# Performance work log

Hardware: AMD Instinct MI355X
Metric: run time of the kernel (lower is better)

Reference implementation:

```python
import jax, jax.numpy as jnp
import numpy as np

T, B, D, H, R, S, M = 1024, 16, 512, 8, 32, 16, 16
TQ = R + T + S   # query length
KL = M + R + T   # key/value length
NEG_INF = -1e8


def setup_inputs() -> dict:
    key = jax.random.key(0)
    ks = jax.random.split(key, 12)
    utterance = jax.random.normal(ks[0], (T, B, D), jnp.float32)
    right_context = jax.random.normal(ks[1], (R, B, D), jnp.float32)
    summary = jax.random.normal(ks[2], (S, B, D), jnp.float32)
    mems = jax.random.normal(ks[3], (M, B, D), jnp.float32)
    # valid lengths in [T//2, T]; force max == T so data-dependent shapes are static
    lengths = jax.random.randint(ks[4], (B,), T // 2, T + 1).at[0].set(T).astype(jnp.int64)
    # block-streaming style mask: query i may only attend to keys <= i + M
    q_idx = jnp.arange(TQ)[:, None]
    k_idx = jnp.arange(KL)[None, :]
    attention_mask = k_idx > (q_idx + M)  # True = masked
    scale = 0.02
    Wq = jax.random.normal(ks[5], (D, D), jnp.float32) * scale
    bq = jnp.zeros((D,), jnp.float32)
    Wkv = jax.random.normal(ks[6], (2 * D, D), jnp.float32) * scale
    bkv = jnp.zeros((2 * D,), jnp.float32)
    Wo = jax.random.normal(ks[7], (D, D), jnp.float32) * scale
    bo = jnp.zeros((D,), jnp.float32)
    return dict(utterance=utterance, lengths=lengths, right_context=right_context,
                summary=summary, mems=mems, attention_mask=attention_mask,
                Wq=Wq, bq=bq, Wkv=Wkv, bkv=bkv, Wo=Wo, bo=bo)


def _split_heads(x):
    # (L, B, D) -> (B*H, L, D//H), matching torch .view(-1, B*H, d).transpose(0, 1)
    L = x.shape[0]
    return x.reshape(L, B * H, D // H).transpose(1, 0, 2)


def reference(utterance, lengths, right_context, summary, mems, attention_mask,
              Wq, bq, Wkv, bkv, Wo, bo):
    d_head = D // H
    scaling = d_head ** -0.5

    query_in = jnp.concatenate([right_context, utterance, summary], axis=0)   # (TQ, B, D)
    kv_in = jnp.concatenate([mems, right_context, utterance], axis=0)         # (KL, B, D)

    query = query_in @ Wq.T + bq
    kv = kv_in @ Wkv.T + bkv
    k, v = jnp.split(kv, 2, axis=2)

    q = _split_heads(query)  # (B*H, TQ, d)
    kh = _split_heads(k)     # (B*H, KL, d)
    vh = _split_heads(v)

    w = jnp.einsum('nqd,nkd->nqk', q * scaling, kh).astype(jnp.float32)
    w = jnp.where(attention_mask[None, :, :], NEG_INF, w)

    # padding mask (B > 1 path): klengths = lengths + M + right_context_blocks_length
    rcbl = TQ - jnp.max(lengths) - S  # == R since max(lengths) == T
    klengths = lengths + M + rcbl
    pad_mask = jnp.arange(KL)[None, :] >= klengths[:, None]  # (B, KL)
    w = w.reshape(B, H, TQ, KL)
    w = jnp.where(pad_mask[:, None, None, :], NEG_INF, w)
    w = w.reshape(B * H, TQ, KL)

    probs = jax.nn.softmax(w, axis=-1)  # dropout p=0.0
    attn = jnp.einsum('nqk,nkd->nqd', probs, vh)          # (B*H, TQ, d)
    attn = attn.transpose(1, 0, 2).reshape(TQ, B, D)

    out = attn @ Wo.T + bo                                # (TQ, B, D)
    output_right_context = out[:TQ - S]                    # (R+T, B, D)
    output_mems = jnp.clip(out[TQ - S:], -10.0, 10.0)      # tanh_on_mem=False
    return output_right_context, output_mems[:-1]          # (S-1, B, D)
```

## Files before the change

### kernel.cpp

```cpp
#include <hip/hip_runtime.h>

#define T_   1024
#define B_   16
#define D_   512
#define H_   8
#define R_   32
#define S_   16
#define M_   16
#define TQ_  1072
#define KL_  1072
#define DH_  64
#define NROW 17152
#define K_   512
#define LQ_  268
#define QSCALE 0.18033688f

typedef unsigned short u16;
using bf16x8 = __attribute__((ext_vector_type(8))) short;
using f32x4  = __attribute__((ext_vector_type(4))) float;
using u16x4  = __attribute__((ext_vector_type(4))) unsigned short;

__device__ __forceinline__ u16 f2bf(float f) {
    unsigned int u = __builtin_bit_cast(unsigned int, f);
    unsigned int r = u + 0x7fffu + ((u >> 16) & 1u);
    return (u16)(r >> 16);
}

__device__ __forceinline__ unsigned int cvt_pk_bf16(float a, float b) {
    unsigned int r;
    asm("v_cvt_pk_bf16_f32 %0, %1, %2" : "=v"(r) : "v"(a), "v"(b));
    return r;
}

__device__ __forceinline__ void gload_lds16(const u16* g, u16* l) {
    __builtin_amdgcn_global_load_lds(
        (const __attribute__((address_space(1))) unsigned int*)g,
        (__attribute__((address_space(3))) unsigned int*)l,
        16, 0, 0);
}

__global__ void k_convert4(const float4* __restrict__ utt, const float4* __restrict__ rc,
                           const float4* __restrict__ smr, const float4* __restrict__ mems,
                           const float4* __restrict__ Wq, const float4* __restrict__ Wkv,
                           const float4* __restrict__ Wo,
                           u16x4* __restrict__ xall,
                           u16x4* __restrict__ wq, u16x4* __restrict__ wkv,
                           u16x4* __restrict__ wo)
{
    const int N4 = 17408 * D_ / 4;
    const int MB = M_ * B_ * D_ / 4;
    const int RB = MB + R_ * B_ * D_ / 4;
    const int UB = RB + T_ * B_ * D_ / 4;
    const int W1 = D_ * D_ / 4, W2 = 2 * D_ * D_ / 4;
    for (int i = blockIdx.x * blockDim.x + threadIdx.x; i < N4;
         i += gridDim.x * blockDim.x) {
        float4 v;
        if (i < MB)      v = mems[i];
        else if (i < RB) v = rc[i - MB];
        else if (i < UB) v = utt[i - RB];
        else             v = smr[i - UB];
        xall[i] = (u16x4){f2bf(v.x), f2bf(v.y), f2bf(v.z), f2bf(v.w)};
        if (i < W1) { v = Wq[i];  wq[i]  = (u16x4){f2bf(v.x), f2bf(v.y), f2bf(v.z), f2bf(v.w)}; }
        if (i < W2) { v = Wkv[i]; wkv[i] = (u16x4){f2bf(v.x), f2bf(v.y), f2bf(v.z), f2bf(v.w)}; }
        if (i < W1) { v = Wo[i];  wo[i]  = (u16x4){f2bf(v.x), f2bf(v.y), f2bf(v.z), f2bf(v.w)}; }
    }
}

#define GEMM_SHARED                                                              \
    __shared__ __align__(16) u16 As[256 * 64];                                   \
    __shared__ __align__(16) u16 Bs[128 * 64];

#define GEMM_PRE(A_PTR, W_PTR)                                                   \
    const int w    = threadIdx.x >> 6;                                           \
    const int lane = threadIdx.x & 63;                                           \
    const int col = lane & 15, quad = lane >> 4;                                 \
    const int lrow = lane >> 3;                                        \
    const int lchk = (lane & 7) ^ lrow;                      \
    const u16* gA = (A_PTR) + (size_t)(tm * 256 + w * 64 + lrow) * K_ + lchk * 8;\
    const u16* gB = (W_PTR) + (size_t)(w * 32 + lrow) * K_ + lchk * 8;

#define GEMM_STAGE(k0)                                                           \
        __syncthreads();                                                         \
        _Pragma("unroll")                                                        \
        for (int i = 0; i < 8; i++)                                              \
            gload_lds16(gA + (k0) + (size_t)i * 8 * K_,                          \
                        &As[(w * 64 + i * 8) * 64]);                             \
        _Pragma("unroll")                                                        \
        for (int j = 0; j < 4; j++)                                              \
            gload_lds16(gB + (k0) + (size_t)j * 8 * K_,                          \
                        &Bs[(w * 32 + j * 8) * 64]);                             \
        __syncthreads();

#define GEMM_FRAGS(kh)                                                           \
            bf16x8 aF[4], bF[8];                                                 \
            _Pragma("unroll")                                                    \
            for (int mi = 0; mi < 4; mi++)                                       \
                aF[mi] = *(const bf16x8*)&As[(w * 64 + mi * 16 + col) * 64       \
                             + ((((kh) * 4 + quad) ^ (col & 7)) * 8)];           \
            _Pragma("unroll")                                                    \
            for (int ni = 0; ni < 8; ni++)                                       \
                bF[ni] = *(const bf16x8*)&Bs[(ni * 16 + col) * 64                \
                             + ((((kh) * 4 + quad) ^ (col & 7)) * 8)];

#define GEMM_CORE(A_PTR, W_PTR)                                                  \
    GEMM_PRE(A_PTR, W_PTR)                                                       \
    f32x4 acc[4][8];                                                             \
    _Pragma("unroll")                                                            \
    for (int mi = 0; mi < 4; mi++)                                               \
        _Pragma("unroll")                                                        \
        for (int ni = 0; ni < 8; ni++) acc[mi][ni] = (f32x4){0.f,0.f,0.f,0.f};   \
    for (int k0 = 0; k0 < K_; k0 += 64) {                                        \
        GEMM_STAGE(k0)                                                           \
        _Pragma("unroll")                                                        \
        for (int kh = 0; kh < 2; kh++) {                                         \
            GEMM_FRAGS(kh)                                                       \
            _Pragma("unroll")                                                    \
            for (int mi = 0; mi < 4; mi++)                                       \
                _Pragma("unroll")                                                \
                for (int ni = 0; ni < 8; ni++)                                   \
                    acc[mi][ni] = __builtin_amdgcn_mfma_f32_16x16x32_bf16(       \
                                      aF[mi], bF[ni], acc[mi][ni], 0, 0, 0);     \
        }                                                                        \
    }

#define GEMM_CORE_T(A_PTR, W_PTR)                                                \
    GEMM_PRE(A_PTR, W_PTR)                                                       \
    f32x4 acc[8][4];                                                             \
    _Pragma("unroll")                                                            \
    for (int ni = 0; ni < 8; ni++)                                               \
        _Pragma("unroll")                                                        \
        for (int mi = 0; mi < 4; mi++) acc[ni][mi] = (f32x4){0.f,0.f,0.f,0.f};   \
    for (int k0 = 0; k0 < K_; k0 += 64) {                                        \
        GEMM_STAGE(k0)                                                           \
        _Pragma("unroll")                                                        \
        for (int kh = 0; kh < 2; kh++) {                                         \
            GEMM_FRAGS(kh)                                                       \
            _Pragma("unroll")                                                    \
            for (int ni = 0; ni < 8; ni++)                                       \
                _Pragma("unroll")                                                \
                for (int mi = 0; mi < 4; mi++)                                   \
                    acc[ni][mi] = __builtin_amdgcn_mfma_f32_16x16x32_bf16(       \
                                      bF[ni], aF[mi], acc[ni][mi], 0, 0, 0);     \
        }                                                                        \
    }

__global__ __launch_bounds__(256, 2)
void k_gemm_qkv(const u16* __restrict__ xall,
                const u16* __restrict__ wqp, const u16* __restrict__ wkvp,
                const float* __restrict__ bq, const float* __restrict__ bkv,
                u16* __restrict__ qb, u16* __restrict__ kb, u16* __restrict__ vt)
{
    const int bid = blockIdx.x;
    const int tn = (bid % 96) >> 3;
    const int tm = (bid / 96) * 8 + (bid & 7);
    if (tm >= 67) return;

    const bool isQ = tn < 4;
    const bool isV = tn >= 8;
    const int wr0 = (isQ ? tn : tn - 4) * 128;
    const u16* Ab = isQ ? (xall + (size_t)256 * K_) : xall;
    const u16* Wb = (isQ ? wqp : wkvp) + (size_t)wr0 * K_;
    const float* bias = isQ ? bq : bkv;

    GEMM_SHARED

    if (isV) {
        GEMM_CORE(Ab, Wb)
#pragma unroll
        for (int ni = 0; ni < 8; ni++) {
            int gcol = wr0 + ni * 16 + col;
            float bs = bias[gcol];
            int f  = gcol - 512;
            int lq = tm * 4 + w;
#pragma unroll
            for (int r = 0; r < 4; r++) {
                int bb = quad * 4 + r;
                uint2 pk;
                pk.x = cvt_pk_bf16(acc[0][ni][r] + bs, acc[1][ni][r] + bs);
                pk.y = cvt_pk_bf16(acc[2][ni][r] + bs, acc[3][ni][r] + bs);
                *(uint2*)&vt[(((size_t)bb * LQ_ + lq) * 512 + f) * 4] = pk;
            }
        }
    } else {
        GEMM_CORE_T(Ab, Wb)
#pragma unroll
        for (int ni = 0; ni < 8; ni++) {
            const int gc0 = wr0 + ni * 16 + quad * 4;
            const float4 bs4 = *(const float4*)&bias[gc0];
#pragma unroll
            for (int mi = 0; mi < 4; mi++) {
                const int mrow = tm * 256 + w * 64 + mi * 16 + col;
                uint2 pk;
                if (isQ) {
                    pk.x = cvt_pk_bf16((acc[ni][mi][0] + bs4.x) * QSCALE,
                                       (acc[ni][mi][1] + bs4.y) * QSCALE);
                    pk.y = cvt_pk_bf16((acc[ni][mi][2] + bs4.z) * QSCALE,
                                       (acc[ni][mi][3] + bs4.w) * QSCALE);
                    *(uint2*)&qb[(size_t)mrow * 512 + gc0] = pk;
                } else {
                    pk.x = cvt_pk_bf16(acc[ni][mi][0] + bs4.x,
                                       acc[ni][mi][1] + bs4.y);
                    pk.y = cvt_pk_bf16(acc[ni][mi][2] + bs4.z,
                                       acc[ni][mi][3] + bs4.w);
                    *(uint2*)&kb[(size_t)mrow * 512 + gc0] = pk;
                }
            }
        }
    }
}

__global__ __launch_bounds__(256, 2)
void k_gemm_o(const u16* __restrict__ A, const u16* __restrict__ W,
              const float* __restrict__ bias, float* __restrict__ Co)
{
    const int bid = blockIdx.x;
    const int tn = (bid % 32) >> 3;
    const int tm = (bid / 32) * 8 + (bid & 7);
    if (tm >= 67) return;

    const u16* Wb = W + (size_t)tn * 128 * K_;

    GEMM_SHARED
    GEMM_CORE_T(A, Wb)

#pragma unroll
    for (int ni = 0; ni < 8; ni++) {
        const int gc0 = tn * 128 + ni * 16 + quad * 4;
        const float4 bs4 = *(const float4*)&bias[gc0];
#pragma unroll
        for (int mi = 0; mi < 4; mi++) {
            const int l = tm * 16 + w * 4 + mi;
            if (l == TQ_ - 1) continue;
            const int mrow = tm * 256 + w * 64 + mi * 16 + col;
            float4 v = {acc[ni][mi][0] + bs4.x, acc[ni][mi][1] + bs4.y,
                        acc[ni][mi][2] + bs4.z, acc[ni][mi][3] + bs4.w};
            if (l >= TQ_ - S_) {
                v.x = fminf(10.0f, fmaxf(-10.0f, v.x));
                v.y = fminf(10.0f, fmaxf(-10.0f, v.y));
                v.z = fminf(10.0f, fmaxf(-10.0f, v.z));
                v.w = fminf(10.0f, fmaxf(-10.0f, v.w));
            }
            *(float4*)&Co[(size_t)mrow * 512 + gc0] = v;
        }
    }
}

__global__ __launch_bounds__(256, 2)
void k_attn5(const u16* __restrict__ qbuf, const u16* __restrict__ kb,
             const u16* __restrict__ vt, const int* __restrict__ lenp,
             u16* __restrict__ attnb)
{
    __shared__ __align__(16) u16 Ks[2][64 * 64];
    __shared__ __align__(16) u16 Vs[2][64 * 64];
    __shared__ __align__(16) u16 Ps[4][16 * 64];

    const int blk  = blockIdx.x;
    const int qblk = 16 - (blk >> 7);
    const int bh   = blk & 127;
    const int b = bh >> 3, h = bh & 7;
    const int tid = threadIdx.x;
    const int w = tid >> 6, lane = tid & 63;
    const int col = lane & 15, quad = lane >> 4;

    int stride = (lenp[1] == 0) ? 2 : 1;
    int maxlen = 0;
    for (int i = 0; i < B_; i++) maxlen = max(maxlen, lenp[i * stride]);
    const int klen = lenp[b * stride] + M_ + (TQ_ - maxlen - S_);

    const int q0 = qblk * 64;
    const int qw = q0 + w * 16;
    const int q  = qw + col;

    int qrow = min(q, TQ_ - 1);
    const u16* qp = qbuf + ((size_t)qrow * B_ + b) * D_ + h * DH_ + quad * 8;
    bf16x8 bq0 = *(const bf16x8*)(qp);
    bf16x8 bq1 = *(const bf16x8*)(qp + 32);

    const int s0 = tid, s1 = tid + 256;
    const u16* kbase = kb + (size_t)b * 512 + h * DH_;
    size_t kof0 = (size_t)(s0 >> 3) * 8192 + (size_t)(((s0 & 7) ^ ((s0 >> 3) & 7)) * 8);
    size_t kof1 = (size_t)(s1 >> 3) * 8192 + (size_t)(((s1 & 7) ^ ((s1 >> 3) & 7)) * 8);
    const u16* vbase = vt + ((size_t)b * LQ_ * 512 + (size_t)h * DH_) * 4;
    auto vchunk = [](int s) -> size_t {
        int fp = s >> 4;
        int lq = (s & 15) ^ (fp & 15);
        return (size_t)lq * 2048 + (size_t)fp * 8;
    };
    const size_t vof0 = vchunk(s0), vof1 = vchunk(s1);

    float li = 0.f;
    f32x4 o[4];
#pragma unroll
    for (int g = 0; g < 4; g++) o[g] = (f32x4){0.f, 0.f, 0.f, 0.f};

    const int nk = min(q0 + 64 + M_, klen);
    const int numkt = (nk + 63) >> 6;
    u16* pw = &Ps[w][0];

    gload_lds16(kbase + kof0, &Ks[0][(size_t)w * 512]);
    gload_lds16(kbase + kof1, &Ks[0][2048 + (size_t)w * 512]);
    gload_lds16(vbase + vof0, &Vs[0][(size_t)w * 512]);
    gload_lds16(vbase + vof1, &Vs[0][2048 + (size_t)w * 512]);

    for (int kt = 0; kt < numkt; kt++) {
        const int kn0 = kt * 64;
        const int cur = kt & 1;
        __syncthreads();
        if (kt + 1 < numkt) {
            const size_t kstep = (size_t)(kn0 + 64) * 8192;
            const size_t vstep = (size_t)(kt + 1) * 32768;
            gload_lds16(kbase + kstep + kof0, &Ks[cur ^ 1][(size_t)w * 512]);
            gload_lds16(kbase + kstep + kof1, &Ks[cur ^ 1][2048 + (size_t)w * 512]);
            gload_lds16(vbase + vstep + vof0, &Vs[cur ^ 1][(size_t)w * 512]);
            gload_lds16(vbase + vstep + vof1, &Vs[cur ^ 1][2048 + (size_t)w * 512]);
        }

        f32x4 sc[4];
        __builtin_amdgcn_s_setprio(1);
#pragma unroll
        for (int g = 0; g < 4; g++) {
            int key = g * 16 + col;
            bf16x8 a0 = *(const bf16x8*)&Ks[cur][key * 64 + ((quad ^ (key & 7)) * 8)];
            bf16x8 a1 = *(const bf16x8*)&Ks[cur][key * 64 + (((4 + quad) ^ (key & 7)) * 8)];
            f32x4 z = {0.f, 0.f, 0.f, 0.f};
            z = __builtin_amdgcn_mfma_f32_16x16x32_bf16(a0, bq0, z, 0, 0, 0);
            z = __builtin_amdgcn_mfma_f32_16x16x32_bf16(a1, bq1, z, 0, 0, 0);
            sc[g] = z;
        }
        __builtin_amdgcn_s_setprio(0);

        const bool needmask = (kn0 + 63 > qw + M_) || (kn0 + 63 >= klen);
        if (needmask) {
#pragma unroll
            for (int g = 0; g < 4; g++)
#pragma unroll
                for (int r = 0; r < 4; r++) {
                    int key = kn0 + g * 16 + quad * 4 + r;
                    bool valid = (key <= q + M_) && (key < klen);
                    sc[g][r] = valid ? sc[g][r] : -1e8f;
                }
        }

#pragma unroll
        for (int g = 0; g < 4; g++) {
            float pr[4];
#pragma unroll
            for (int r = 0; r < 4; r++) {
                pr[r] = __builtin_amdgcn_exp2f(sc[g][r]);
                li += pr[r];
            }
            uint2 pk;
            pk.x = cvt_pk_bf16(pr[0], pr[1]);
            pk.y = cvt_pk_bf16(pr[2], pr[3]);
            int kc = g * 2 + (quad >> 1);
            *(uint2*)&pw[col * 64 + ((kc ^ (col & 7)) * 8) + (quad & 1) * 4] = pk;
        }

        bf16x8 ap0 = *(const bf16x8*)&pw[col * 64 + ((quad ^ (col & 7)) * 8)];
        bf16x8 ap1 = *(const bf16x8*)&pw[col * 64 + (((4 + quad) ^ (col & 7)) * 8)];
        __builtin_amdgcn_s_setprio(1);
#pragma unroll
        for (int g = 0; g < 4; g++) {
            int d = g * 16 + col;
            int fp = d >> 1, fo = (d & 1) * 4;
            bf16x8 bv[2];
#pragma unroll
            for (int hh = 0; hh < 2; hh++) {
                int lqA = hh * 8 + quad * 2;
                int posA = fp * 16 + (lqA ^ (fp & 15));
                int posB = fp * 16 + ((lqA + 1) ^ (fp & 15));
                u16x4 loA = *(const u16x4*)&Vs[cur][posA * 8 + fo];
                u16x4 loB = *(const u16x4*)&Vs[cur][posB * 8 + fo];
                bf16x8 t;
                t[0] = loA[0]; t[1] = loA[1]; t[2] = loA[2]; t[3] = loA[3];
                t[4] = loB[0]; t[5] = loB[1]; t[6] = loB[2]; t[7] = loB[3];
                bv[hh] = t;
            }
            o[g] = __builtin_amdgcn_mfma_f32_16x16x32_bf16(bv[0], ap0, o[g], 0, 0, 0);
            o[g] = __builtin_amdgcn_mfma_f32_16x16x32_bf16(bv[1], ap1, o[g], 0, 0, 0);
        }
        __builtin_amdgcn_s_setprio(0);
    }

    li += __shfl_xor(li, 16);
    li += __shfl_xor(li, 32);
    const float inv = 1.0f / li;
    const int qo = qw + col;
    if (qw + 16 <= TQ_) {
#pragma unroll
        for (int g = 0; g < 4; g++) {
            uint2 pk;
            pk.x = cvt_pk_bf16(o[g][0] * inv, o[g][1] * inv);
            pk.y = cvt_pk_bf16(o[g][2] * inv, o[g][3] * inv);
            *(uint2*)&attnb[((size_t)qo * B_ + b) * D_ + h * DH_ + g * 16 + quad * 4] = pk;
        }
    }
}

extern "C" void kernel_launch(void* const* d_in, const int* in_sizes, int n_in,
                              void* d_out, int out_size, void* d_ws, size_t ws_size,
                              hipStream_t stream)
{
    const float* utt  = (const float*)d_in[0];
    const int*   len  = (const int*)  d_in[1];
    const float* rc   = (const float*)d_in[2];
    const float* smr  = (const float*)d_in[3];
    const float* mems = (const float*)d_in[4];
    const float* Wq   = (const float*)d_in[6];
    const float* bq   = (const float*)d_in[7];
    const float* Wkv  = (const float*)d_in[8];
    const float* bkv  = (const float*)d_in[9];
    const float* Wo   = (const float*)d_in[10];
    const float* bo   = (const float*)d_in[11];

    char* ws = (char*)d_ws;
    size_t off = 0;
    auto alloc = [&](size_t bytes) -> void* {
        void* p = ws + off;
        off += (bytes + 255) & ~(size_t)255;
        return p;
    };
    u16* xall = (u16*)alloc((size_t)17408 * D_ * 2);
    u16* wq   = (u16*)alloc((size_t)D_ * D_ * 2);
    u16* wkv  = (u16*)alloc((size_t)2 * D_ * D_ * 2);
    u16* wo   = (u16*)alloc((size_t)D_ * D_ * 2);
    u16* qb   = (u16*)alloc((size_t)NROW * D_ * 2);
    u16* kb   = (u16*)alloc((size_t)NROW * D_ * 2);
    u16* vt   = (u16*)alloc((size_t)B_ * LQ_ * 512 * 4 * 2 + 65536);
    u16* attnb = xall;

    k_convert4<<<2048, 256, 0, stream>>>((const float4*)utt, (const float4*)rc,
                                         (const float4*)smr, (const float4*)mems,
                                         (const float4*)Wq, (const float4*)Wkv,
                                         (const float4*)Wo,
                                         (u16x4*)xall,
                                         (u16x4*)wq, (u16x4*)wkv, (u16x4*)wo);
    k_gemm_qkv<<<9 * 96, 256, 0, stream>>>(xall, wq, wkv, bq, bkv, qb, kb, vt);
    k_attn5<<<17 * 128, 256, 0, stream>>>(qb, kb, vt, len, attnb);
    k_gemm_o<<<9 * 32, 256, 0, stream>>>(attnb, wo, bo, (float*)d_out);
}
```

Before: 215.6 us.

## Rewrite projection GEMMs with double-buffered LDS pipeline and 8-wave 256x256 tiles

Both projection GEMMs move from a single-buffered 256x128 tile with 4 waves to a templated core that double-buffers A/B tiles in dynamic LDS and issues the next stage's loads before computing the current one. Blocks grow to 8 waves with 256x256 (QKV) or 128x256 (output) tiles, and MFMA sections are wrapped in s_setprio. The goal is to hide global-load latency behind MFMA work and cut redundant tile loads. In exchange it uses 128KB/96KB of LDS per block, which limits occupancy, and launches fewer blocks for the QKV GEMM (402).

```diff
diff --git a/kernel.cpp b/kernel.cpp
--- a/kernel.cpp
+++ b/kernel.cpp
@@ -66,174 +66,172 @@
     }
 }
 
-#define GEMM_SHARED                                                              \
-    __shared__ __align__(16) u16 As[256 * 64];                                   \
-    __shared__ __align__(16) u16 Bs[128 * 64];
-
-#define GEMM_PRE(A_PTR, W_PTR)                                                   \
-    const int w    = threadIdx.x >> 6;                                           \
-    const int lane = threadIdx.x & 63;                                           \
-    const int col = lane & 15, quad = lane >> 4;                                 \
-    const int lrow = lane >> 3;                                        \
-    const int lchk = (lane & 7) ^ lrow;                      \
-    const u16* gA = (A_PTR) + (size_t)(tm * 256 + w * 64 + lrow) * K_ + lchk * 8;\
-    const u16* gB = (W_PTR) + (size_t)(w * 32 + lrow) * K_ + lchk * 8;
-
-#define GEMM_STAGE(k0)                                                           \
-        __syncthreads();                                                         \
-        _Pragma("unroll")                                                        \
-        for (int i = 0; i < 8; i++)                                              \
-            gload_lds16(gA + (k0) + (size_t)i * 8 * K_,                          \
-                        &As[(w * 64 + i * 8) * 64]);                             \
-        _Pragma("unroll")                                                        \
-        for (int j = 0; j < 4; j++)                                              \
-            gload_lds16(gB + (k0) + (size_t)j * 8 * K_,                          \
-                        &Bs[(w * 32 + j * 8) * 64]);                             \
+template<int MREP, bool TOR>
+__device__ __forceinline__ void pipe_core(const u16* __restrict__ Ab,
+                                          const u16* __restrict__ Wb,
+                                          u16* lds, f32x4* acc)
+{
+    const int BM = MREP * 32;
+    u16* As0 = lds;
+    u16* As1 = lds + BM * 64;
+    u16* Bs0 = lds + 2 * BM * 64;
+    u16* Bs1 = lds + 2 * BM * 64 + 256 * 64;
+
+    const int tid  = threadIdx.x;
+    const int wid  = tid >> 6, lane = tid & 63;
+    const int wm   = wid >> 2, wn = wid & 3;
+    const int col  = lane & 15, quad = lane >> 4;
+    const int sr   = tid >> 3;
+    const int sc   = (tid & 7) ^ (sr & 7);
+    const u16* gA  = Ab + (size_t)sr * K_ + sc * 8;
+    const u16* gB  = Wb + (size_t)sr * K_ + sc * 8;
+
+#pragma unroll
+    for (int i = 0; i < MREP * 4; i++) acc[i] = (f32x4){0.f, 0.f, 0.f, 0.f};
+
+    auto stage = [&](int kt, u16* Au, u16* Bu) {
+#pragma unroll
+        for (int i = 0; i < MREP / 2; i++)
+            gload_lds16(gA + (size_t)(i * 64) * K_ + kt * 64,
+                        Au + (i * 64 + wid * 8) * 64);
+#pragma unroll
+        for (int i = 0; i < 4; i++)
+            gload_lds16(gB + (size_t)(i * 64) * K_ + kt * 64,
+                        Bu + (i * 64 + wid * 8) * 64);
+    };
+
+    stage(0, As0, Bs0);
+    __syncthreads();
+
+    u16 *Ac = As0, *Bc = Bs0, *An = As1, *Bn = Bs1;
+    for (int kt = 0; kt < 8; ++kt) {
+        if (kt < 7) stage(kt + 1, An, Bn);
+#pragma unroll
+        for (int kh = 0; kh < 2; ++kh) {
+            bf16x8 aF[MREP], bF[4];
+#pragma unroll
+            for (int mi = 0; mi < MREP; mi++)
+                aF[mi] = *(const bf16x8*)&Ac[(wm * (MREP * 16) + mi * 16 + col) * 64
+                             + (((kh * 4 + quad) ^ (col & 7)) * 8)];
+#pragma unroll
+            for (int ni = 0; ni < 4; ni++)
+                bF[ni] = *(const bf16x8*)&Bc[(wn * 64 + ni * 16 + col) * 64
+                             + (((kh * 4 + quad) ^ (col & 7)) * 8)];
+            __builtin_amdgcn_s_setprio(1);
+            if (TOR) {
+#pragma unroll
+                for (int ni = 0; ni < 4; ni++)
+#pragma unroll
+                    for (int mi = 0; mi < MREP; mi++)
+                        acc[ni * MREP + mi] = __builtin_amdgcn_mfma_f32_16x16x32_bf16(
+                            bF[ni], aF[mi], acc[ni * MREP + mi], 0, 0, 0);
+            } else {
+#pragma unroll
+                for (int mi = 0; mi < MREP; mi++)
+#pragma unroll
+                    for (int ni = 0; ni < 4; ni++)
+                        acc[mi * 4 + ni] = __builtin_amdgcn_mfma_f32_16x16x32_bf16(
+                            aF[mi], bF[ni], acc[mi * 4 + ni], 0, 0, 0);
+            }
+            __builtin_amdgcn_s_setprio(0);
+        }
         __syncthreads();
-
-#define GEMM_FRAGS(kh)                                                           \
-            bf16x8 aF[4], bF[8];                                                 \
-            _Pragma("unroll")                                                    \
-            for (int mi = 0; mi < 4; mi++)                                       \
-                aF[mi] = *(const bf16x8*)&As[(w * 64 + mi * 16 + col) * 64       \
-                             + ((((kh) * 4 + quad) ^ (col & 7)) * 8)];           \
-            _Pragma("unroll")                                                    \
-            for (int ni = 0; ni < 8; ni++)                                       \
-                bF[ni] = *(const bf16x8*)&Bs[(ni * 16 + col) * 64                \
-                             + ((((kh) * 4 + quad) ^ (col & 7)) * 8)];
-
-#define GEMM_CORE(A_PTR, W_PTR)                                                  \
-    GEMM_PRE(A_PTR, W_PTR)                                                       \
-    f32x4 acc[4][8];                                                             \
-    _Pragma("unroll")                                                            \
-    for (int mi = 0; mi < 4; mi++)                                               \
-        _Pragma("unroll")                                                        \
-        for (int ni = 0; ni < 8; ni++) acc[mi][ni] = (f32x4){0.f,0.f,0.f,0.f};   \
-    for (int k0 = 0; k0 < K_; k0 += 64) {                                        \
-        GEMM_STAGE(k0)                                                           \
-        _Pragma("unroll")                                                        \
-        for (int kh = 0; kh < 2; kh++) {                                         \
-            GEMM_FRAGS(kh)                                                       \
-            _Pragma("unroll")                                                    \
-            for (int mi = 0; mi < 4; mi++)                                       \
-                _Pragma("unroll")                                                \
-                for (int ni = 0; ni < 8; ni++)                                   \
-                    acc[mi][ni] = __builtin_amdgcn_mfma_f32_16x16x32_bf16(       \
-                                      aF[mi], bF[ni], acc[mi][ni], 0, 0, 0);     \
-        }                                                                        \
-    }
-
-#define GEMM_CORE_T(A_PTR, W_PTR)                                                \
-    GEMM_PRE(A_PTR, W_PTR)                                                       \
-    f32x4 acc[8][4];                                                             \
-    _Pragma("unroll")                                                            \
-    for (int ni = 0; ni < 8; ni++)                                               \
-        _Pragma("unroll")                                                        \
-        for (int mi = 0; mi < 4; mi++) acc[ni][mi] = (f32x4){0.f,0.f,0.f,0.f};   \
-    for (int k0 = 0; k0 < K_; k0 += 64) {                                        \
-        GEMM_STAGE(k0)                                                           \
-        _Pragma("unroll")                                                        \
-        for (int kh = 0; kh < 2; kh++) {                                         \
-            GEMM_FRAGS(kh)                                                       \
-            _Pragma("unroll")                                                    \
-            for (int ni = 0; ni < 8; ni++)                                       \
-                _Pragma("unroll")                                                \
-                for (int mi = 0; mi < 4; mi++)                                   \
-                    acc[ni][mi] = __builtin_amdgcn_mfma_f32_16x16x32_bf16(       \
-                                      bF[ni], aF[mi], acc[ni][mi], 0, 0, 0);     \
-        }                                                                        \
-    }
-
-__global__ __launch_bounds__(256, 2)
-void k_gemm_qkv(const u16* __restrict__ xall,
-                const u16* __restrict__ wqp, const u16* __restrict__ wkvp,
-                const float* __restrict__ bq, const float* __restrict__ bkv,
-                u16* __restrict__ qb, u16* __restrict__ kb, u16* __restrict__ vt)
-{
+        u16* t;
+        t = Ac; Ac = An; An = t;
+        t = Bc; Bc = Bn; Bn = t;
+    }
+}
+
+__global__ __launch_bounds__(512, 2)
+void k_gemm_qkv8(const u16* __restrict__ xall,
+                 const u16* __restrict__ wqp, const u16* __restrict__ wkvp,
+                 const float* __restrict__ bq, const float* __restrict__ bkv,
+                 u16* __restrict__ qb, u16* __restrict__ kb, u16* __restrict__ vt)
+{
+    extern __shared__ u16 lds[];
     const int bid = blockIdx.x;
-    const int tn = (bid % 96) >> 3;
-    const int tm = (bid / 96) * 8 + (bid & 7);
-    if (tm >= 67) return;
-
-    const bool isQ = tn < 4;
-    const bool isV = tn >= 8;
-    const int wr0 = (isQ ? tn : tn - 4) * 128;
-    const u16* Ab = isQ ? (xall + (size_t)256 * K_) : xall;
-    const u16* Wb = (isQ ? wqp : wkvp) + (size_t)wr0 * K_;
-    const float* bias = isQ ? bq : bkv;
-
-    GEMM_SHARED
-
-    if (isV) {
-        GEMM_CORE(Ab, Wb)
-#pragma unroll
-        for (int ni = 0; ni < 8; ni++) {
-            int gcol = wr0 + ni * 16 + col;
-            float bs = bias[gcol];
-            int f  = gcol - 512;
-            int lq = tm * 4 + w;
-#pragma unroll
-            for (int r = 0; r < 4; r++) {
-                int bb = quad * 4 + r;
+    const int tn = bid % 6, tm = bid / 6;
+    const int typ = tn >> 1, half = tn & 1;
+    const u16* Ab = (typ == 0 ? xall + (size_t)256 * K_ : xall)
+                    + (size_t)tm * 256 * K_;
+    const u16* Wb = (typ == 0 ? wqp : wkvp + (typ == 2 ? (size_t)512 * K_ : 0))
+                    + (size_t)half * 256 * K_;
+
+    const int wid = threadIdx.x >> 6, lane = threadIdx.x & 63;
+    const int wm = wid >> 2, wn = wid & 3;
+    const int col = lane & 15, quad = lane >> 4;
+
+    f32x4 acc[32];
+    if (typ == 2) {
+        pipe_core<8, false>(Ab, Wb, lds, acc);
+#pragma unroll
+        for (int ni = 0; ni < 4; ni++) {
+            const int f = half * 256 + wn * 64 + ni * 16 + col;
+            const float bs = bkv[512 + f];
+#pragma unroll
+            for (int mg = 0; mg < 2; mg++) {
+                const int lq = tm * 4 + wm * 2 + mg;
+#pragma unroll
+                for (int r = 0; r < 4; r++) {
+                    const int bb = quad * 4 + r;
+                    uint2 pk;
+                    pk.x = cvt_pk_bf16(acc[(mg * 4 + 0) * 4 + ni][r] + bs,
+                                       acc[(mg * 4 + 1) * 4 + ni][r] + bs);
+                    pk.y = cvt_pk_bf16(acc[(mg * 4 + 2) * 4 + ni][r] + bs,
+                                       acc[(mg * 4 + 3) * 4 + ni][r] + bs);
+                    *(uint2*)&vt[(((size_t)bb * LQ_ + lq) * 512 + f) * 4] = pk;
+                }
+            }
+        }
+    } else {
+        pipe_core<8, true>(Ab, Wb, lds, acc);
+        const float* bias = (typ == 0) ? bq : bkv;
+        u16* outp = (typ == 0) ? qb : kb;
+        const float qs = (typ == 0) ? QSCALE : 1.0f;
+#pragma unroll
+        for (int ni = 0; ni < 4; ni++) {
+            const int gc0 = half * 256 + wn * 64 + ni * 16 + quad * 4;
+            const float4 bs4 = *(const float4*)&bias[gc0];
+#pragma unroll
+            for (int mi = 0; mi < 8; mi++) {
+                const int mrow = tm * 256 + wm * 128 + mi * 16 + col;
+                f32x4 a = acc[ni * 8 + mi];
                 uint2 pk;
-                pk.x = cvt_pk_bf16(acc[0][ni][r] + bs, acc[1][ni][r] + bs);
-                pk.y = cvt_pk_bf16(acc[2][ni][r] + bs, acc[3][ni][r] + bs);
-                *(uint2*)&vt[(((size_t)bb * LQ_ + lq) * 512 + f) * 4] = pk;
-            }
-        }
-    } else {
-        GEMM_CORE_T(Ab, Wb)
-#pragma unroll
-        for (int ni = 0; ni < 8; ni++) {
-            const int gc0 = wr0 + ni * 16 + quad * 4;
-            const float4 bs4 = *(const float4*)&bias[gc0];
-#pragma unroll
-            for (int mi = 0; mi < 4; mi++) {
-                const int mrow = tm * 256 + w * 64 + mi * 16 + col;
-                uint2 pk;
-                if (isQ) {
-                    pk.x = cvt_pk_bf16((acc[ni][mi][0] + bs4.x) * QSCALE,
-                                       (acc[ni][mi][1] + bs4.y) * QSCALE);
-                    pk.y = cvt_pk_bf16((acc[ni][mi][2] + bs4.z) * QSCALE,
-                                       (acc[ni][mi][3] + bs4.w) * QSCALE);
-                    *(uint2*)&qb[(size_t)mrow * 512 + gc0] = pk;
-                } else {
-                    pk.x = cvt_pk_bf16(acc[ni][mi][0] + bs4.x,
-                                       acc[ni][mi][1] + bs4.y);
-                    pk.y = cvt_pk_bf16(acc[ni][mi][2] + bs4.z,
-                                       acc[ni][mi][3] + bs4.w);
-                    *(uint2*)&kb[(size_t)mrow * 512 + gc0] = pk;
-                }
-            }
-        }
-    }
-}
-
-__global__ __launch_bounds__(256, 2)
-void k_gemm_o(const u16* __restrict__ A, const u16* __restrict__ W,
-              const float* __restrict__ bias, float* __restrict__ Co)
-{
-    const int bid = blockIdx.x;
-    const int tn = (bid % 32) >> 3;
-    const int tm = (bid / 32) * 8 + (bid & 7);
-    if (tm >= 67) return;
-
-    const u16* Wb = W + (size_t)tn * 128 * K_;
-
-    GEMM_SHARED
-    GEMM_CORE_T(A, Wb)
-
-#pragma unroll
-    for (int ni = 0; ni < 8; ni++) {
-        const int gc0 = tn * 128 + ni * 16 + quad * 4;
+                pk.x = cvt_pk_bf16((a[0] + bs4.x) * qs, (a[1] + bs4.y) * qs);
+                pk.y = cvt_pk_bf16((a[2] + bs4.z) * qs, (a[3] + bs4.w) * qs);
+                *(uint2*)&outp[(size_t)mrow * 512 + gc0] = pk;
+            }
+        }
+    }
+}
+
+__global__ __launch_bounds__(512, 2)
+void k_gemm_o8(const u16* __restrict__ A, const u16* __restrict__ W,
+               const float* __restrict__ bias, float* __restrict__ Co)
+{
+    extern __shared__ u16 lds[];
+    const int tn = blockIdx.x % 2, tm = blockIdx.x / 2;
+    const u16* Ab = A + (size_t)tm * 128 * K_;
+    const u16* Wb = W + (size_t)tn * 256 * K_;
+
+    const int wid = threadIdx.x >> 6, lane = threadIdx.x & 63;
+    const int wm = wid >> 2, wn = wid & 3;
+    const int col = lane & 15, quad = lane >> 4;
+
+    f32x4 acc[16];
+    pipe_core<4, true>(Ab, Wb, lds, acc);
+
+#pragma unroll
+    for (int ni = 0; ni < 4; ni++) {
+        const int gc0 = tn * 256 + wn * 64 + ni * 16 + quad * 4;
         const float4 bs4 = *(const float4*)&bias[gc0];
 #pragma unroll
         for (int mi = 0; mi < 4; mi++) {
-            const int l = tm * 16 + w * 4 + mi;
+            const int l = tm * 8 + wm * 4 + mi;
             if (l == TQ_ - 1) continue;
-            const int mrow = tm * 256 + w * 64 + mi * 16 + col;
-            float4 v = {acc[ni][mi][0] + bs4.x, acc[ni][mi][1] + bs4.y,
-                        acc[ni][mi][2] + bs4.z, acc[ni][mi][3] + bs4.w};
+            const int mrow = tm * 128 + wm * 64 + mi * 16 + col;
+            f32x4 a = acc[ni * 4 + mi];
+            float4 v = {a[0] + bs4.x, a[1] + bs4.y, a[2] + bs4.z, a[3] + bs4.w};
             if (l >= TQ_ - S_) {
                 v.x = fminf(10.0f, fmaxf(-10.0f, v.x));
                 v.y = fminf(10.0f, fmaxf(-10.0f, v.y));
@@ -429,13 +427,22 @@
     u16* vt   = (u16*)alloc((size_t)B_ * LQ_ * 512 * 4 * 2 + 65536);
     u16* attnb = xall;
 
+    static int s_attr_done = 0;
+    if (!s_attr_done) {
+        hipFuncSetAttribute(reinterpret_cast<const void*>(k_gemm_qkv8),
+                            hipFuncAttributeMaxDynamicSharedMemorySize, 131072);
+        hipFuncSetAttribute(reinterpret_cast<const void*>(k_gemm_o8),
+                            hipFuncAttributeMaxDynamicSharedMemorySize, 98304);
+        s_attr_done = 1;
+    }
+
     k_convert4<<<2048, 256, 0, stream>>>((const float4*)utt, (const float4*)rc,
                                          (const float4*)smr, (const float4*)mems,
                                          (const float4*)Wq, (const float4*)Wkv,
                                          (const float4*)Wo,
                                          (u16x4*)xall,
                                          (u16x4*)wq, (u16x4*)wkv, (u16x4*)wo);
-    k_gemm_qkv<<<9 * 96, 256, 0, stream>>>(xall, wq, wkv, bq, bkv, qb, kb, vt);
+    k_gemm_qkv8<<<67 * 6, 512, 131072, stream>>>(xall, wq, wkv, bq, bkv, qb, kb, vt);
     k_attn5<<<17 * 128, 256, 0, stream>>>(qb, kb, vt, len, attnb);
-    k_gemm_o<<<9 * 32, 256, 0, stream>>>(attnb, wo, bo, (float*)d_out);
-}
+    k_gemm_o8<<<134 * 2, 512, 98304, stream>>>(attnb, wo, bo, (float*)d_out);
+}
```

Result: slower. 221.6 us (+2.8%).
